# Kernel optimization log

Hardware: AMD Instinct MI355X
Metric: run time of the kernel (lower is better)

The kernel has to match this reference:

```python
import jax, jax.numpy as jnp
import numpy as np

N, M, D, S = 4, 256, 32, 32


def setup_inputs() -> dict:
    key = jax.random.key(0)
    k1, k2 = jax.random.split(key)
    inputs = jax.random.normal(k1, (N, M, M, D), dtype=jnp.float32)
    mask = jnp.ones((N, M, 1), dtype=bool)
    coeffs = jax.random.normal(k2, (D, S, 15), dtype=jnp.float32) * np.sqrt(2.0) / (D + S)
    diag_bias = jnp.zeros((1, S, 1, 1), dtype=jnp.float32)
    all_bias = jnp.zeros((1, S, 1, 1), dtype=jnp.float32)
    return {"inputs": inputs, "mask": mask, "coeffs": coeffs,
            "diag_bias": diag_bias, "all_bias": all_bias}


def _contractions_2_to_2(x):
    # x: [N, D, m, m]; returns list of 15 [N, D, m, m] basis tensors ('inf' normalization)
    n, d, m, _ = x.shape
    diag = jnp.diagonal(x, axis1=2, axis2=3)            # [N, D, m]
    sum_diag = jnp.sum(diag, axis=2, keepdims=True)      # [N, D, 1]
    rows = jnp.sum(x, axis=3)                            # [N, D, m]
    cols = jnp.sum(x, axis=2)                            # [N, D, m]
    tot = jnp.sum(rows, axis=2)                          # [N, D]
    eye = jnp.eye(m, dtype=x.dtype)

    def diag_embed(v):  # v: [N, D, m] -> [N, D, m, m]
        return v[..., :, None] * eye

    full = x.shape
    op1 = diag_embed(diag)
    op2 = diag_embed(jnp.broadcast_to(sum_diag, diag.shape)) / m
    op3 = diag_embed(rows) / m
    op4 = diag_embed(cols) / m
    op5 = diag_embed(jnp.broadcast_to(tot[..., None], diag.shape)) / (m ** 2)
    op6 = jnp.broadcast_to(cols[..., :, None], full) / m
    op7 = jnp.broadcast_to(rows[..., :, None], full) / m
    op8 = jnp.broadcast_to(cols[..., None, :], full) / m
    op9 = jnp.broadcast_to(rows[..., None, :], full) / m
    op10 = x
    op11 = jnp.swapaxes(x, 2, 3)
    op12 = jnp.broadcast_to(diag[..., :, None], full)
    op13 = jnp.broadcast_to(diag[..., None, :], full)
    op14 = jnp.broadcast_to(sum_diag[..., None], full) / m
    op15 = jnp.broadcast_to(tot[..., None, None], full) / (m ** 2)
    return [op1, op2, op3, op4, op5, op6, op7, op8, op9, op10,
            op11, op12, op13, op14, op15]


def reference(inputs, mask, coeffs, diag_bias, all_bias):
    # inputs: [N, m, m, D] -> [N, D, m, m]
    x = jnp.transpose(inputs, (0, 3, 1, 2))
    m = x.shape[3]
    ops = _contractions_2_to_2(x)
    # einsum('dsb,ndbij->nsij') expressed as accumulation over the 15 bases
    # (avoids materializing the [N, D, 15, m, m] stack)
    out = jnp.zeros((x.shape[0], coeffs.shape[1], m, m), dtype=x.dtype)
    for b, op in enumerate(ops):
        out = out + jnp.einsum('ds,ndij->nsij', coeffs[:, :, b], op)
    eye = jnp.eye(m, dtype=x.dtype)[None, None]
    out = out + all_bias + eye * diag_bias
    return jnp.transpose(out, (0, 2, 3, 1))  # [N, m, m, S]
```

## Files before the change

### kernel.cpp

```cpp
#include <hip/hip_runtime.h>


#define NN 4
#define MM 256
#define DD 32
#define SS 32

#define WS_COLSP  0
#define WS_ROWS   262144
#define WS_DIAG   294912
#define WS_SD     327680
#define WS_TOT    327808
#define WS_RW     327936
#define WS_CWT4   360704
#define WS_DW     393472
#define WS_CPACK  426240

__global__ __launch_bounds__(256) void k_reduce(const float* __restrict__ in,
                                                const float* __restrict__ coeffs,
                                                float* __restrict__ ws) {
    int blk = blockIdx.x;
    int t = threadIdx.x;
    if (blk < 256) {
        int n = blk >> 6, rem = blk & 63, jb = rem >> 3, ie = rem & 7;
        int i0 = ie * 32, j0 = jb * 32;
        int jl = t >> 3, d4 = t & 7;
        const float4* base = (const float4*)in
            + ((size_t)(n * MM + i0) * MM + j0 + jl) * 8 + d4;
        float4 a = {0.f, 0.f, 0.f, 0.f};
        #pragma unroll 8
        for (int i = 0; i < 32; ++i) {
            float4 v = base[(size_t)i * MM * 8];
            a.x += v.x; a.y += v.y; a.z += v.z; a.w += v.w;
        }
        ((float4*)(ws + WS_COLSP))[(size_t)ie * 8192 + (n * MM + j0 + jl) * 8 + d4] = a;
    } else if (blk < 256 + NN * MM) {
        int nm = blk - 256;
        int n = nm >> 8;
        int ii = nm & 255;
        const float4* base = (const float4*)(in + (size_t)nm * MM * DD);
        float4 a = {0.f, 0.f, 0.f, 0.f};
        #pragma unroll
        for (int k = 0; k < 8; ++k) {
            float4 v = base[t + k * 256];
            a.x += v.x; a.y += v.y; a.z += v.z; a.w += v.w;
        }
        __shared__ float4 red[256];
        red[t] = a;
        __syncthreads();
        if (t < 8) {
            float4 s = {0.f, 0.f, 0.f, 0.f};
            #pragma unroll 8
            for (int g = 0; g < 32; ++g) {
                float4 v = red[g * 8 + t];
                s.x += v.x; s.y += v.y; s.z += v.z; s.w += v.w;
            }
            ((float4*)(ws + WS_ROWS))[nm * 8 + t] = s;
            float4 dv = ((const float4*)in)[((size_t)nm * MM + ii) * 8 + t];
            ((float4*)(ws + WS_DIAG))[nm * 8 + t] = dv;
            atomicAdd(ws + WS_TOT + n * DD + t * 4 + 0, s.x);
            atomicAdd(ws + WS_TOT + n * DD + t * 4 + 1, s.y);
            atomicAdd(ws + WS_TOT + n * DD + t * 4 + 2, s.z);
            atomicAdd(ws + WS_TOT + n * DD + t * 4 + 3, s.w);
            atomicAdd(ws + WS_SD + n * DD + t * 4 + 0, dv.x);
            atomicAdd(ws + WS_SD + n * DD + t * 4 + 1, dv.y);
            atomicAdd(ws + WS_SD + n * DD + t * 4 + 2, dv.z);
            atomicAdd(ws + WS_SD + n * DD + t * 4 + 3, dv.w);
        }
    } else {
        for (int idx = t; idx < 15 * DD * SS; idx += 256) {
            int plane = idx >> 10;
            int ds = idx & 1023;
            ws[WS_CPACK + plane * (DD * SS) + ds] = coeffs[ds * 15 + plane];
        }
    }
}

__global__ __launch_bounds__(256) void k_aux(const float* __restrict__ diag_bias,
                                             const float* __restrict__ all_bias,
                                             float* __restrict__ ws) {
    int idx = blockIdx.x * blockDim.x + threadIdx.x;
    int s = idx & 31;
    int nm = idx >> 5;
    int n = nm >> 8;
    int m = nm & 255;
    const float inv_m = 1.0f / MM;
    const float inv_m2 = inv_m * inv_m;
    float u = 0.f, v = 0.f, dgacc = 0.f, w = 0.f;
    for (int d = 0; d < DD; ++d) {
        const float* cp = ws + WS_CPACK + d * SS + s;
        float r = ws[WS_ROWS + nm * DD + d];
        float cl = 0.f;
        #pragma unroll
        for (int q = 0; q < 8; ++q) cl += ws[WS_COLSP + q * 32768 + nm * DD + d];
        float dv = ws[WS_DIAG + nm * DD + d];
        float sdv = ws[WS_SD + n * DD + d];
        float totv = ws[WS_TOT + n * DD + d];
        u += cp[5 * 1024] * cl * inv_m + cp[6 * 1024] * r * inv_m + cp[11 * 1024] * dv;
        v += cp[7 * 1024] * cl * inv_m + cp[8 * 1024] * r * inv_m + cp[12 * 1024] * dv;
        dgacc += cp[0] * dv + cp[1 * 1024] * sdv * inv_m + cp[2 * 1024] * r * inv_m
               + cp[3 * 1024] * cl * inv_m + cp[4 * 1024] * totv * inv_m2;
        w += cp[13 * 1024] * sdv * inv_m + cp[14 * 1024] * totv * inv_m2;
    }
    ws[WS_RW + nm * SS + s] = u + w + all_bias[s];
    ws[WS_CWT4 + (((n * 8 + (s >> 2)) * MM + m) << 2) + (s & 3)] = v;
    ws[WS_DW + nm * SS + s] = dgacc + diag_bias[s];
}

__global__ __launch_bounds__(256) void k_main(const float* __restrict__ in,
                                              const float* __restrict__ ws,
                                              float* __restrict__ out) {
    __shared__ float tile[256 * 36];
    int nm = blockIdx.x;
    int n = nm >> 8;
    int i = nm & 255;
    int t = threadIdx.x;

    const float4* Arow = (const float4*)(in + (size_t)nm * MM * DD);
    float4 avv[8];
    #pragma unroll
    for (int k = 0; k < 8; ++k) avv[k] = Arow[t + k * 256];

    float4 cvv[8];
    const float4* cwt4 = (const float4*)(ws + WS_CWT4) + (size_t)n * 8 * MM + t;
    #pragma unroll
    for (int sq = 0; sq < 8; ++sq) cvv[sq] = cwt4[sq * MM];
    float4 dvv[8] = {};
    if (t == i) {
        const float4* dw = (const float4*)(ws + WS_DW + nm * SS);
        #pragma unroll
        for (int q = 0; q < 8; ++q) dvv[q] = dw[q];
    }

    const float4* Bbase = (const float4*)in;
    float4 bvv[8];
    #pragma unroll
    for (int k = 0; k < 8; ++k) {
        int idx = t + k * 256;
        int p = idx >> 3, c = idx & 7;
        bvv[k] = Bbase[((size_t)(n * MM + p) * MM + i) * 8 + c];
    }
    __builtin_amdgcn_sched_barrier(0);

    #pragma unroll
    for (int k = 0; k < 8; ++k) {
        int idx = t + k * 256;
        int p = idx >> 3, c = idx & 7;
        *(float4*)(tile + p * 36 + c * 4) = avv[k];
    }
    __syncthreads();

    const float* rwp = ws + WS_RW + nm * SS;
    float acc[SS];
    #pragma unroll
    for (int sq = 0; sq < 8; ++sq) {
        acc[sq * 4 + 0] = rwp[sq * 4 + 0] + cvv[sq].x + dvv[sq].x;
        acc[sq * 4 + 1] = rwp[sq * 4 + 1] + cvv[sq].y + dvv[sq].y;
        acc[sq * 4 + 2] = rwp[sq * 4 + 2] + cvv[sq].z + dvv[sq].z;
        acc[sq * 4 + 3] = rwp[sq * 4 + 3] + cvv[sq].w + dvv[sq].w;
    }

    const float* c10 = ws + WS_CPACK + 9 * (DD * SS);
    const float* c11 = ws + WS_CPACK + 10 * (DD * SS);
    const float* lrow = tile + t * 36;
    #pragma unroll
    for (int dq = 0; dq < 8; ++dq) {
        float4 a4 = *(const float4*)(lrow + dq * 4);
        const float* ca = c10 + dq * 4 * SS;
        #pragma unroll
        for (int r = 0; r < 4; ++r) {
            float a = (r == 0) ? a4.x : (r == 1) ? a4.y : (r == 2) ? a4.z : a4.w;
            #pragma unroll
            for (int s = 0; s < SS; ++s)
                acc[s] = fmaf(a, ca[r * SS + s], acc[s]);
        }
    }
    __syncthreads();

    #pragma unroll
    for (int k = 0; k < 8; ++k) {
        int idx = t + k * 256;
        int p = idx >> 3, c = idx & 7;
        *(float4*)(tile + p * 36 + c * 4) = bvv[k];
    }
    __syncthreads();

    #pragma unroll
    for (int dq = 0; dq < 8; ++dq) {
        float4 b4 = *(const float4*)(lrow + dq * 4);
        const float* cb = c11 + dq * 4 * SS;
        #pragma unroll
        for (int r = 0; r < 4; ++r) {
            float bb = (r == 0) ? b4.x : (r == 1) ? b4.y : (r == 2) ? b4.z : b4.w;
            #pragma unroll
            for (int s = 0; s < SS; ++s)
                acc[s] = fmaf(bb, cb[r * SS + s], acc[s]);
        }
    }
    #pragma unroll
    for (int q = 0; q < 8; ++q)
        *(float4*)(tile + t * 36 + q * 4) =
            make_float4(acc[q * 4 + 0], acc[q * 4 + 1], acc[q * 4 + 2], acc[q * 4 + 3]);
    __syncthreads();

    float4* Orow = (float4*)(out + (size_t)nm * MM * SS);
    #pragma unroll
    for (int k = 0; k < 8; ++k) {
        int idx = t + k * 256;
        int p = idx >> 3, c = idx & 7;
        Orow[idx] = *(const float4*)(tile + p * 36 + c * 4);
    }
}

extern "C" void kernel_launch(void* const* d_in, const int* in_sizes, int n_in,
                              void* d_out, int out_size, void* d_ws, size_t ws_size,
                              hipStream_t stream) {
    const float* in = (const float*)d_in[0];
    const float* coeffs = (const float*)d_in[2];
    const float* diag_bias = (const float*)d_in[3];
    const float* all_bias = (const float*)d_in[4];
    float* out = (float*)d_out;
    float* ws = (float*)d_ws;

    hipMemsetAsync((char*)d_ws + (size_t)WS_SD * 4, 0, 256 * sizeof(float), stream);
    k_reduce<<<256 + NN * MM + 1, 256, 0, stream>>>(in, coeffs, ws);
    k_aux<<<(NN * MM * SS) / 256, 256, 0, stream>>>(diag_bias, all_bias, ws);
    k_main<<<NN * MM, 256, 0, stream>>>(in, ws, out);
}
```

Measured before the change: 165.9 us.

## Remove LDS staging in main kernel; per-thread direct row loads with 64-thread blocks

Rewrites the main kernel so each thread handles one output (i,j) position and loads its A and B 32-float rows directly into registers, eliminating the shared-memory transpose tile and all block barriers. The grid becomes four 64-thread blocks per row with a launch bound favoring registers. This removes LDS traffic and synchronization, at the cost of strided, less coalesced per-lane global loads and stores and possibly lower occupancy.

```diff
diff --git a/kernel.cpp b/kernel.cpp
--- a/kernel.cpp
+++ b/kernel.cpp
@@ -107,109 +107,87 @@
     ws[WS_DW + nm * SS + s] = dgacc + diag_bias[s];
 }
 
-__global__ __launch_bounds__(256) void k_main(const float* __restrict__ in,
-                                              const float* __restrict__ ws,
-                                              float* __restrict__ out) {
-    __shared__ float tile[256 * 36];
-    int nm = blockIdx.x;
+__global__ __launch_bounds__(64, 3) void k_main(const float* __restrict__ in,
+                                                const float* __restrict__ ws,
+                                                float* __restrict__ out) {
+    int b = blockIdx.x;
+    int jq = b & 3;
+    int nm = b >> 2;
     int n = nm >> 8;
     int i = nm & 255;
-    int t = threadIdx.x;
-
-    const float4* Arow = (const float4*)(in + (size_t)nm * MM * DD);
-    float4 avv[8];
-    #pragma unroll
-    for (int k = 0; k < 8; ++k) avv[k] = Arow[t + k * 256];
-
+    int j = jq * 64 + threadIdx.x;
+
+    const float4* A = (const float4*)(in + ((size_t)nm * MM + j) * DD);
+    float4 av[8];
+    #pragma unroll
+    for (int k = 0; k < 8; ++k) av[k] = A[k];
+
+    const float4* B = (const float4*)(in + ((size_t)(n * MM + j) * MM + i) * DD);
+    float4 bv[8];
+    #pragma unroll
+    for (int k = 0; k < 8; ++k) bv[k] = B[k];
+
+    const float4* cwt4 = (const float4*)(ws + WS_CWT4) + (size_t)n * 8 * MM + j;
     float4 cvv[8];
-    const float4* cwt4 = (const float4*)(ws + WS_CWT4) + (size_t)n * 8 * MM + t;
     #pragma unroll
     for (int sq = 0; sq < 8; ++sq) cvv[sq] = cwt4[sq * MM];
-    float4 dvv[8] = {};
-    if (t == i) {
-        const float4* dw = (const float4*)(ws + WS_DW + nm * SS);
-        #pragma unroll
-        for (int q = 0; q < 8; ++q) dvv[q] = dw[q];
-    }
-
-    const float4* Bbase = (const float4*)in;
-    float4 bvv[8];
-    #pragma unroll
-    for (int k = 0; k < 8; ++k) {
-        int idx = t + k * 256;
-        int p = idx >> 3, c = idx & 7;
-        bvv[k] = Bbase[((size_t)(n * MM + p) * MM + i) * 8 + c];
-    }
-    __builtin_amdgcn_sched_barrier(0);
-
-    #pragma unroll
-    for (int k = 0; k < 8; ++k) {
-        int idx = t + k * 256;
-        int p = idx >> 3, c = idx & 7;
-        *(float4*)(tile + p * 36 + c * 4) = avv[k];
-    }
-    __syncthreads();
 
     const float* rwp = ws + WS_RW + nm * SS;
     float acc[SS];
     #pragma unroll
-    for (int sq = 0; sq < 8; ++sq) {
-        acc[sq * 4 + 0] = rwp[sq * 4 + 0] + cvv[sq].x + dvv[sq].x;
-        acc[sq * 4 + 1] = rwp[sq * 4 + 1] + cvv[sq].y + dvv[sq].y;
-        acc[sq * 4 + 2] = rwp[sq * 4 + 2] + cvv[sq].z + dvv[sq].z;
-        acc[sq * 4 + 3] = rwp[sq * 4 + 3] + cvv[sq].w + dvv[sq].w;
-    }
+    for (int s = 0; s < SS; ++s) acc[s] = rwp[s];
 
     const float* c10 = ws + WS_CPACK + 9 * (DD * SS);
     const float* c11 = ws + WS_CPACK + 10 * (DD * SS);
-    const float* lrow = tile + t * 36;
+
     #pragma unroll
     for (int dq = 0; dq < 8; ++dq) {
-        float4 a4 = *(const float4*)(lrow + dq * 4);
         const float* ca = c10 + dq * 4 * SS;
         #pragma unroll
         for (int r = 0; r < 4; ++r) {
-            float a = (r == 0) ? a4.x : (r == 1) ? a4.y : (r == 2) ? a4.z : a4.w;
+            float a = (r == 0) ? av[dq].x : (r == 1) ? av[dq].y : (r == 2) ? av[dq].z : av[dq].w;
             #pragma unroll
             for (int s = 0; s < SS; ++s)
                 acc[s] = fmaf(a, ca[r * SS + s], acc[s]);
         }
     }
-    __syncthreads();
-
-    #pragma unroll
-    for (int k = 0; k < 8; ++k) {
-        int idx = t + k * 256;
-        int p = idx >> 3, c = idx & 7;
-        *(float4*)(tile + p * 36 + c * 4) = bvv[k];
-    }
-    __syncthreads();
 
     #pragma unroll
     for (int dq = 0; dq < 8; ++dq) {
-        float4 b4 = *(const float4*)(lrow + dq * 4);
         const float* cb = c11 + dq * 4 * SS;
         #pragma unroll
         for (int r = 0; r < 4; ++r) {
-            float bb = (r == 0) ? b4.x : (r == 1) ? b4.y : (r == 2) ? b4.z : b4.w;
+            float bb = (r == 0) ? bv[dq].x : (r == 1) ? bv[dq].y : (r == 2) ? bv[dq].z : bv[dq].w;
             #pragma unroll
             for (int s = 0; s < SS; ++s)
                 acc[s] = fmaf(bb, cb[r * SS + s], acc[s]);
         }
     }
+
+    #pragma unroll
+    for (int sq = 0; sq < 8; ++sq) {
+        acc[sq * 4 + 0] += cvv[sq].x;
+        acc[sq * 4 + 1] += cvv[sq].y;
+        acc[sq * 4 + 2] += cvv[sq].z;
+        acc[sq * 4 + 3] += cvv[sq].w;
+    }
+
+    if (j == i) {
+        const float4* dw = (const float4*)(ws + WS_DW + nm * SS);
+        #pragma unroll
+        for (int q = 0; q < 8; ++q) {
+            float4 dq = dw[q];
+            acc[q * 4 + 0] += dq.x;
+            acc[q * 4 + 1] += dq.y;
+            acc[q * 4 + 2] += dq.z;
+            acc[q * 4 + 3] += dq.w;
+        }
+    }
+
+    float4* O = (float4*)(out + ((size_t)nm * MM + j) * SS);
     #pragma unroll
     for (int q = 0; q < 8; ++q)
-        *(float4*)(tile + t * 36 + q * 4) =
-            make_float4(acc[q * 4 + 0], acc[q * 4 + 1], acc[q * 4 + 2], acc[q * 4 + 3]);
-    __syncthreads();
-
-    float4* Orow = (float4*)(out + (size_t)nm * MM * SS);
-    #pragma unroll
-    for (int k = 0; k < 8; ++k) {
-        int idx = t + k * 256;
-        int p = idx >> 3, c = idx & 7;
-        Orow[idx] = *(const float4*)(tile + p * 36 + c * 4);
-    }
+        O[q] = make_float4(acc[q * 4 + 0], acc[q * 4 + 1], acc[q * 4 + 2], acc[q * 4 + 3]);
 }
 
 extern "C" void kernel_launch(void* const* d_in, const int* in_sizes, int n_in,
@@ -225,5 +203,5 @@
     hipMemsetAsync((char*)d_ws + (size_t)WS_SD * 4, 0, 256 * sizeof(float), stream);
     k_reduce<<<256 + NN * MM + 1, 256, 0, stream>>>(in, coeffs, ws);
     k_aux<<<(NN * MM * SS) / 256, 256, 0, stream>>>(diag_bias, all_bias, ws);
-    k_main<<<NN * MM, 256, 0, stream>>>(in, ws, out);
-}
+    k_main<<<NN * MM * 4, 64, 0, stream>>>(in, ws, out);
+}
```

After: 170.8 us. 3.0% more time.
